# Kernel optimization log

Measured on AMD Instinct MI355X. Metric: run time of the kernel, lower is better.

The kernel has to match this reference:

```python
import jax, jax.numpy as jnp
import numpy as np

SOFTMAX_TEMP = 0.01  # config['networks']['matcher_block']['softmax_temp']
B, WINDOW, C, N, WIDTH = 2, 2, 64, 400, 256


def setup_inputs() -> dict:
    key = jax.random.key(0)
    k1, k2, k3 = jax.random.split(key, 3)
    BW = B * WINDOW
    keypoint_scores = jax.random.uniform(k1, (BW, 1, N), dtype=jnp.float32)
    keypoint_desc = jax.random.normal(k2, (BW, C, N), dtype=jnp.float32)
    desc_dense = jax.random.normal(k3, (BW, C, WIDTH, WIDTH), dtype=jnp.float32)
    # pairing indices exactly as built in SoftmaxRefMatcher.__init__
    tgt_ids, src_ids = [], []
    for b in range(B):
        for w in range(WINDOW - 1):
            for t in range(w + 1, WINDOW):
                src_ids.append(w + b * WINDOW)
                tgt_ids.append(t + b * WINDOW)
    return {
        "keypoint_scores": keypoint_scores,
        "keypoint_desc": keypoint_desc,
        "desc_dense": desc_dense,
        "tgt_ids": jnp.array(tgt_ids, dtype=jnp.int32),
        "src_ids": jnp.array(src_ids, dtype=jnp.int32),
    }


def _l2_normalize(x):
    # F.normalize(x, dim=1), eps=1e-12
    return x / jnp.maximum(jnp.linalg.norm(x, axis=1, keepdims=True), 1e-12)


def reference(keypoint_scores, keypoint_desc, desc_dense, tgt_ids, src_ids):
    BW, Cdim, H, W = desc_dense.shape
    HW = H * W
    # src_coords_dense: meshgrid('ij') -> coords[k] = (u=k%W, v=k//W)
    hw = jnp.arange(HW)
    coords = jnp.stack([(hw % W).astype(jnp.float32),
                        (hw // W).astype(jnp.float32)], axis=1)  # [HW, 2]

    src_desc = _l2_normalize(desc_dense.reshape(BW, Cdim, HW))[src_ids]  # [P, C, HW]
    tgt_desc = _l2_normalize(keypoint_desc)[tgt_ids]                     # [P, C, N]

    match_vals = jnp.einsum('pcn,pcm->pnm', tgt_desc, src_desc)          # [P, N, HW]
    soft_match = jax.nn.softmax(match_vals / SOFTMAX_TEMP, axis=2)
    pseudo_coords = jnp.einsum('pnm,mk->pnk', soft_match, coords)        # [P, N, 2]

    tgt_scores = keypoint_scores[tgt_ids]
    return pseudo_coords, tgt_scores, tgt_ids, src_ids
```

## Files before the change

### kernel.cpp

```cpp
#include <hip/hip_runtime.h>
#include <math.h>

#define NPAIR  2
#define KDIM   64
#define NKP    400
#define NTILE  28
#define HWPIX  65536
#define MREF   70.0f
#define LOG2E  1.44269504f

#define BFRAG_DW (NPAIR*NTILE*2*2*256)

using frag_ab = __attribute__((ext_vector_type(8))) short;
using f32x4   = __attribute__((ext_vector_type(4))) float;

__device__ __forceinline__ unsigned short f2bf(float f){
    unsigned u = __builtin_bit_cast(unsigned, f);
    u += 0x7fffu + ((u >> 16) & 1u);
    return (unsigned short)(u >> 16);
}
__device__ __forceinline__ float bf2f(unsigned short h){
    unsigned u = ((unsigned)h) << 16;
    return __builtin_bit_cast(float, u);
}

__global__ __launch_bounds__(256) void prep_kernel(
    const float* __restrict__ ksc, const float* __restrict__ kd,
    const int* __restrict__ tgt_ids, const int* __restrict__ src_ids,
    unsigned* __restrict__ wsu, float* __restrict__ out)
{
    __shared__ float xs[KDIM][33];
    __shared__ float inv_s[32];
    int d = blockIdx.x, p = blockIdx.y, t = threadIdx.x;
    int tgt = tgt_ids[p];
    int nl = t & 31, c0 = t >> 5;
    #pragma unroll
    for (int cc = 0; cc < 8; ++cc){
        int c = cc*8 + c0;
        int n = d*32 + nl;
        xs[c][nl] = (n < NKP) ? kd[(tgt*KDIM + c)*NKP + n] : 0.f;
    }
    __syncthreads();
    if (t < 32){
        float s = 0.f;
        #pragma unroll
        for (int c = 0; c < KDIM; ++c){ float v = xs[c][t]; s = fmaf(v, v, s); }
        inv_s[t] = 1.f / fmaxf(sqrtf(s), 1e-12f);
    }
    __syncthreads();
    {
        int l = t & 63, rk = t >> 6;
        int rt = rk >> 1, ks = rk & 1;
        int cl = l & 15, g = l >> 4;
        int nloc = rt*16 + cl;
        float inv = inv_s[nloc];
        int k0 = ks*32 + g*8;
        unsigned hu[4], lu[4];
        #pragma unroll
        for (int j2 = 0; j2 < 4; ++j2){
            float xa = xs[k0 + 2*j2    ][nloc] * inv;
            float xb = xs[k0 + 2*j2 + 1][nloc] * inv;
            unsigned short ha = f2bf(xa), hb = f2bf(xb);
            unsigned short la = f2bf(xa - bf2f(ha)), lb = f2bf(xb - bf2f(hb));
            hu[j2] = (unsigned)ha | ((unsigned)hb << 16);
            lu[j2] = (unsigned)la | ((unsigned)lb << 16);
        }
        int nt = d*2 + rt;
        unsigned base = (unsigned)(((p*NTILE + nt)*2 + ks)*2)*256 + l*4;
        *(uint4*)&wsu[base]       = make_uint4(hu[0], hu[1], hu[2], hu[3]);
        *(uint4*)&wsu[base + 256] = make_uint4(lu[0], lu[1], lu[2], lu[3]);
    }
    if (t < 32){
        int n = d*32 + t;
        if (n < NKP) out[NPAIR*NKP*2 + p*NKP + n] = ksc[tgt*NKP + n];
    }
    if (d == 0 && t == 0){
        out[NPAIR*NKP*3 + p]         = (float)tgt;
        out[NPAIR*NKP*3 + NPAIR + p] = (float)src_ids[p];
    }
}

__global__ __launch_bounds__(256, 4) void match_kernel(
    const float* __restrict__ dd, const int* __restrict__ src_ids,
    const unsigned* __restrict__ wsu, float* __restrict__ part)
{
    __shared__ unsigned lds[8192];
    __shared__ float ssp[256];
    __shared__ float invn_s[128];
    int mb = blockIdx.x, p = blockIdx.y, t = threadIdx.x;
    int w = t >> 6, l = t & 63;
    int g = l >> 4;

    const unsigned* wB = wsu + (unsigned)p*28672 + (unsigned)l*4;
    uint4 Bb0[4], Bb1[4];
    #pragma unroll
    for (int k = 0; k < 4; ++k) Bb0[k] = *(const uint4*)(wB + k*256);
    #pragma unroll
    for (int k = 0; k < 4; ++k) Bb1[k] = *(const uint4*)(wB + 1024 + k*256);

    const float* plane = dd + (size_t)src_ids[p]*KDIM*HWPIX + mb*128;

    {
        int m = t & 127, kh = t >> 7;
        unsigned sw = (unsigned)(m & 7);
        float ssum = 0.f;
        const float* cp = plane + m + (size_t)kh*32*HWPIX;
        #pragma unroll
        for (int s2l = 0; s2l < 4; ++s2l){
            float v[8];
            #pragma unroll
            for (int j = 0; j < 8; ++j) v[j] = cp[(size_t)(s2l*8 + j)*HWPIX];
            unsigned hq[4], lq[4];
            #pragma unroll
            for (int q = 0; q < 4; ++q){
                float a = v[2*q], b = v[2*q+1];
                ssum = fmaf(a, a, ssum);
                ssum = fmaf(b, b, ssum);
                unsigned ta = (__builtin_bit_cast(unsigned, a) + 0x8000u) & 0xFFFF0000u;
                unsigned tb = (__builtin_bit_cast(unsigned, b) + 0x8000u) & 0xFFFF0000u;
                float la = a - __builtin_bit_cast(float, ta);
                float lb = b - __builtin_bit_cast(float, tb);
                hq[q] = __builtin_amdgcn_perm(tb, ta, 0x07060302u);
                lq[q] = __builtin_amdgcn_perm(__builtin_bit_cast(unsigned, lb),
                                              __builtin_bit_cast(unsigned, la), 0x07060302u);
            }
            unsigned slot = ((unsigned)(kh*4 + s2l)) ^ sw;
            unsigned dwb = (unsigned)m*32 + slot*4;
            *(uint4*)&lds[dwb]        = make_uint4(hq[0], hq[1], hq[2], hq[3]);
            *(uint4*)&lds[4096 + dwb] = make_uint4(lq[0], lq[1], lq[2], lq[3]);
        }
        ssp[t] = ssum;
    }
    __syncthreads();
    if (t < 128)
        invn_s[t] = (100.f * LOG2E) / fmaxf(sqrtf(ssp[t] + ssp[t + 128]), 1e-12f);
    __syncthreads();

    int mloc0 = w*32;
    uint4 Ac[2][4];
    #pragma unroll
    for (int mt = 0; mt < 2; ++mt){
        unsigned m = (unsigned)(mloc0 + mt*16 + (l & 15));
        unsigned sw = m & 7;
        #pragma unroll
        for (int k = 0; k < 4; ++k){
            unsigned slot = (((unsigned)(k >> 1))*4 + (unsigned)g) ^ sw;
            Ac[mt][k] = *(const uint4*)&lds[(unsigned)(k & 1)*4096 + m*32 + slot*4];
        }
    }
    __syncthreads();

    const float mref2 = MREF * LOG2E;
    float invm8[2][4], ub_[2];
    #pragma unroll
    for (int mt = 0; mt < 2; ++mt){
        ub_[mt] = (float)(mloc0 + mt*16 + g*4);
        #pragma unroll
        for (int r = 0; r < 4; ++r)
            invm8[mt][r] = invn_s[mloc0 + mt*16 + g*4 + r];
    }

    f32x4 acc0[2], acc1[2];
    float* wp = (float*)lds;

    auto zacc = [&](f32x4* a){
        a[0] = (f32x4){0.f,0.f,0.f,0.f};
        a[1] = (f32x4){0.f,0.f,0.f,0.f};
    };
    auto unit = [&](const uint4* Bq, f32x4* a2){
        #pragma unroll
        for (int ks = 0; ks < 2; ++ks){
            frag_ab bH  = __builtin_bit_cast(frag_ab, Bq[ks*2]);
            frag_ab bL  = __builtin_bit_cast(frag_ab, Bq[ks*2 + 1]);
            frag_ab a0H = __builtin_bit_cast(frag_ab, Ac[0][ks*2]);
            frag_ab a0L = __builtin_bit_cast(frag_ab, Ac[0][ks*2 + 1]);
            frag_ab a1H = __builtin_bit_cast(frag_ab, Ac[1][ks*2]);
            frag_ab a1L = __builtin_bit_cast(frag_ab, Ac[1][ks*2 + 1]);
            a2[0] = __builtin_amdgcn_mfma_f32_16x16x32_bf16(a0H, bH, a2[0], 0, 0, 0);
            a2[1] = __builtin_amdgcn_mfma_f32_16x16x32_bf16(a1H, bH, a2[1], 0, 0, 0);
            a2[0] = __builtin_amdgcn_mfma_f32_16x16x32_bf16(a0H, bL, a2[0], 0, 0, 0);
            a2[1] = __builtin_amdgcn_mfma_f32_16x16x32_bf16(a1H, bL, a2[1], 0, 0, 0);
            a2[0] = __builtin_amdgcn_mfma_f32_16x16x32_bf16(a0L, bH, a2[0], 0, 0, 0);
            a2[1] = __builtin_amdgcn_mfma_f32_16x16x32_bf16(a1L, bH, a2[1], 0, 0, 0);
        }
    };
    auto loadB = [&](int nt, uint4* B){
        const unsigned* q = wB + (unsigned)nt*1024;
        #pragma unroll
        for (int k = 0; k < 4; ++k) B[k] = *(const uint4*)(q + k*256);
    };
    auto epi = [&](const f32x4* a2, int nt){
        float Ssum = 0.f, Usum = 0.f;
        #pragma unroll
        for (int mt = 0; mt < 2; ++mt){
            float e0 = __builtin_amdgcn_exp2f(fmaf(a2[mt][0], invm8[mt][0], -mref2));
            float e1 = __builtin_amdgcn_exp2f(fmaf(a2[mt][1], invm8[mt][1], -mref2));
            float e2 = __builtin_amdgcn_exp2f(fmaf(a2[mt][2], invm8[mt][2], -mref2));
            float e3 = __builtin_amdgcn_exp2f(fmaf(a2[mt][3], invm8[mt][3], -mref2));
            float Sm = (e0 + e1) + (e2 + e3);
            float Um = fmaf(e2, 2.f, e1);
            Um = fmaf(e3, 3.f, Um);
            Um = fmaf(ub_[mt], Sm, Um);
            Ssum += Sm; Usum += Um;
        }
        Ssum += __shfl_xor(Ssum, 16); Usum += __shfl_xor(Usum, 16);
        Ssum += __shfl_xor(Ssum, 32); Usum += __shfl_xor(Usum, 32);
        if (l < 16)
            *(float2*)&wp[((unsigned)(w*NTILE + nt)*16 + (unsigned)l)*2] =
                make_float2(Ssum, Usum);
    };

    zacc(acc0); unit(Bb0, acc0);
    #pragma unroll 1
    for (int j = 0; j < 13; ++j){
        loadB(2*j + 2, Bb0);
        zacc(acc1); unit(Bb1, acc1);
        epi(acc0, 2*j);
        loadB(2*j + 3, Bb1);
        zacc(acc0); unit(Bb0, acc0);
        epi(acc1, 2*j + 1);
    }
    zacc(acc1); unit(Bb1, acc1);
    epi(acc0, 26);
    epi(acc1, 27);

    __syncthreads();
    for (int idx = t; idx < NTILE*16; idx += 256){
        int nt = idx >> 4, cl = idx & 15;
        float S = 0.f, U = 0.f;
        #pragma unroll
        for (int ww = 0; ww < 4; ++ww){
            float2 q = *(const float2*)&wp[((unsigned)(ww*NTILE + nt)*16 + (unsigned)cl)*2];
            S += q.x; U += q.y;
        }
        *(float2*)&part[(((size_t)p*NTILE + nt)*512 + mb)*32 + cl*2] =
            make_float2(S, U);
    }
}

__global__ __launch_bounds__(256) void merge_kernel(
    const float* __restrict__ part, float* __restrict__ out)
{
    __shared__ float red[3][4][16];
    int nt = blockIdx.x, p = blockIdx.y, t = threadIdx.x;
    int j = t & 15, mb0 = t >> 4;
    const float* base = part + ((size_t)(p*NTILE + nt)*512)*32;
    float S = 0.f, U = 0.f, V = 0.f;
    #pragma unroll 4
    for (int k = 0; k < 32; ++k){
        int mbk = mb0 + k*16;
        float2 q = *(const float2*)&base[(mbk*16 + j)*2];
        S += q.x;
        U += q.y + (float)((mbk & 1)*128)*q.x;
        V = fmaf((float)(mbk >> 1), q.x, V);
    }
    S += __shfl_xor(S, 16); U += __shfl_xor(U, 16); V += __shfl_xor(V, 16);
    S += __shfl_xor(S, 32); U += __shfl_xor(U, 32); V += __shfl_xor(V, 32);
    int w = t >> 6, l = t & 63;
    if (l < 16){ red[0][w][j] = S; red[1][w][j] = U; red[2][w][j] = V; }
    __syncthreads();
    if (t < 16){
        float Sf = red[0][0][t] + red[0][1][t] + red[0][2][t] + red[0][3][t];
        float Uf = red[1][0][t] + red[1][1][t] + red[1][2][t] + red[1][3][t];
        float Vf = red[2][0][t] + red[2][1][t] + red[2][2][t] + red[2][3][t];
        int n = nt*16 + t;
        out[(p*NKP + n)*2 + 0] = Uf / Sf;
        out[(p*NKP + n)*2 + 1] = Vf / Sf;
    }
}

extern "C" void kernel_launch(void* const* d_in, const int* in_sizes, int n_in,
                              void* d_out, int out_size, void* d_ws, size_t ws_size,
                              hipStream_t stream)
{
    const float* ksc     = (const float*)d_in[0];
    const float* kd      = (const float*)d_in[1];
    const float* dd      = (const float*)d_in[2];
    const int*   tgt_ids = (const int*)d_in[3];
    const int*   src_ids = (const int*)d_in[4];
    float* out = (float*)d_out;
    unsigned* wsu = (unsigned*)d_ws;
    float* part = (float*)d_ws + BFRAG_DW;

    prep_kernel <<<dim3(14, NPAIR),  256, 0, stream>>>(ksc, kd, tgt_ids, src_ids, wsu, out);
    match_kernel<<<dim3(512, NPAIR), 256, 0, stream>>>(dd, src_ids, wsu, part);
    merge_kernel<<<dim3(25, NPAIR),  256, 0, stream>>>(part, out);
}
```

Baseline: 127.0 us.

## Double pixels per match block so each B fragment load feeds four M tiles

Each match block now covers 256 pixels (one full image row) instead of 128. Each wave holds four 16-row A tiles instead of two, so every B fragment loaded from the workspace is reused across twice as many MFMAs. The number of blocks and partial sums halves, and the merge kernel is simplified to match the new row-per-block indexing. In exchange, register pressure rises (launch bounds drop to 2 blocks per SIMD), occupancy falls, and the grid shrinks to 512 blocks total, which may reduce latency hiding on the HBM-bound load phase.

```diff
diff --git a/kernel.cpp b/kernel.cpp
--- a/kernel.cpp
+++ b/kernel.cpp
@@ -8,6 +8,7 @@
 #define HWPIX  65536
 #define MREF   70.0f
 #define LOG2E  1.44269504f
+#define MBLK   256
 
 #define BFRAG_DW (NPAIR*NTILE*2*2*256)
 
@@ -80,13 +81,13 @@
     }
 }
 
-__global__ __launch_bounds__(256, 4) void match_kernel(
+__global__ __launch_bounds__(256, 2) void match_kernel(
     const float* __restrict__ dd, const int* __restrict__ src_ids,
     const unsigned* __restrict__ wsu, float* __restrict__ part)
 {
     __shared__ unsigned lds[8192];
     __shared__ float ssp[256];
-    __shared__ float invn_s[128];
+    __shared__ float invn_s[256];
     int mb = blockIdx.x, p = blockIdx.y, t = threadIdx.x;
     int w = t >> 6, l = t & 63;
     int g = l >> 4;
@@ -98,13 +99,15 @@
     #pragma unroll
     for (int k = 0; k < 4; ++k) Bb1[k] = *(const uint4*)(wB + 1024 + k*256);
 
-    const float* plane = dd + (size_t)src_ids[p]*KDIM*HWPIX + mb*128;
-
-    {
-        int m = t & 127, kh = t >> 7;
+    const float* plane = dd + (size_t)src_ids[p]*KDIM*HWPIX + (size_t)mb*256;
+
+    uint4 Ac[4][4];
+    int m = t & 127, kh = t >> 7;
+    #pragma unroll
+    for (int chunk = 0; chunk < 2; ++chunk){
         unsigned sw = (unsigned)(m & 7);
         float ssum = 0.f;
-        const float* cp = plane + m + (size_t)kh*32*HWPIX;
+        const float* cp = plane + chunk*128 + m + (size_t)kh*32*HWPIX;
         #pragma unroll
         for (int s2l = 0; s2l < 4; ++s2l){
             float v[8];
@@ -130,58 +133,64 @@
             *(uint4*)&lds[4096 + dwb] = make_uint4(lq[0], lq[1], lq[2], lq[3]);
         }
         ssp[t] = ssum;
-    }
-    __syncthreads();
-    if (t < 128)
-        invn_s[t] = (100.f * LOG2E) / fmaxf(sqrtf(ssp[t] + ssp[t + 128]), 1e-12f);
-    __syncthreads();
-
-    int mloc0 = w*32;
-    uint4 Ac[2][4];
-    #pragma unroll
-    for (int mt = 0; mt < 2; ++mt){
-        unsigned m = (unsigned)(mloc0 + mt*16 + (l & 15));
-        unsigned sw = m & 7;
-        #pragma unroll
-        for (int k = 0; k < 4; ++k){
-            unsigned slot = (((unsigned)(k >> 1))*4 + (unsigned)g) ^ sw;
-            Ac[mt][k] = *(const uint4*)&lds[(unsigned)(k & 1)*4096 + m*32 + slot*4];
-        }
-    }
-    __syncthreads();
+        __syncthreads();
+        if (t < 128)
+            invn_s[chunk*128 + t] =
+                (100.f * LOG2E) / fmaxf(sqrtf(ssp[t] + ssp[t + 128]), 1e-12f);
+        if ((w >> 1) == chunk){
+            int lw = (w & 1)*64;
+            #pragma unroll
+            for (int mt = 0; mt < 4; ++mt){
+                unsigned mm = (unsigned)(lw + mt*16 + (l & 15));
+                unsigned sw2 = mm & 7;
+                #pragma unroll
+                for (int k = 0; k < 4; ++k){
+                    unsigned slot = (((unsigned)(k >> 1))*4 + (unsigned)g) ^ sw2;
+                    Ac[mt][k] = *(const uint4*)&lds[(unsigned)(k & 1)*4096 + mm*32 + slot*4];
+                }
+            }
+        }
+        __syncthreads();
+    }
 
     const float mref2 = MREF * LOG2E;
-    float invm8[2][4], ub_[2];
-    #pragma unroll
-    for (int mt = 0; mt < 2; ++mt){
+    float invm8[4][4], ub_[4];
+    int mloc0 = w*64;
+    #pragma unroll
+    for (int mt = 0; mt < 4; ++mt){
         ub_[mt] = (float)(mloc0 + mt*16 + g*4);
         #pragma unroll
         for (int r = 0; r < 4; ++r)
             invm8[mt][r] = invn_s[mloc0 + mt*16 + g*4 + r];
     }
 
-    f32x4 acc0[2], acc1[2];
+    f32x4 acc0[4], acc1[4];
     float* wp = (float*)lds;
 
     auto zacc = [&](f32x4* a){
-        a[0] = (f32x4){0.f,0.f,0.f,0.f};
-        a[1] = (f32x4){0.f,0.f,0.f,0.f};
-    };
-    auto unit = [&](const uint4* Bq, f32x4* a2){
+        #pragma unroll
+        for (int mt = 0; mt < 4; ++mt) a[mt] = (f32x4){0.f,0.f,0.f,0.f};
+    };
+    auto unit = [&](const uint4* Bq, f32x4* a4){
         #pragma unroll
         for (int ks = 0; ks < 2; ++ks){
-            frag_ab bH  = __builtin_bit_cast(frag_ab, Bq[ks*2]);
-            frag_ab bL  = __builtin_bit_cast(frag_ab, Bq[ks*2 + 1]);
-            frag_ab a0H = __builtin_bit_cast(frag_ab, Ac[0][ks*2]);
-            frag_ab a0L = __builtin_bit_cast(frag_ab, Ac[0][ks*2 + 1]);
-            frag_ab a1H = __builtin_bit_cast(frag_ab, Ac[1][ks*2]);
-            frag_ab a1L = __builtin_bit_cast(frag_ab, Ac[1][ks*2 + 1]);
-            a2[0] = __builtin_amdgcn_mfma_f32_16x16x32_bf16(a0H, bH, a2[0], 0, 0, 0);
-            a2[1] = __builtin_amdgcn_mfma_f32_16x16x32_bf16(a1H, bH, a2[1], 0, 0, 0);
-            a2[0] = __builtin_amdgcn_mfma_f32_16x16x32_bf16(a0H, bL, a2[0], 0, 0, 0);
-            a2[1] = __builtin_amdgcn_mfma_f32_16x16x32_bf16(a1H, bL, a2[1], 0, 0, 0);
-            a2[0] = __builtin_amdgcn_mfma_f32_16x16x32_bf16(a0L, bH, a2[0], 0, 0, 0);
-            a2[1] = __builtin_amdgcn_mfma_f32_16x16x32_bf16(a1L, bH, a2[1], 0, 0, 0);
+            frag_ab bH = __builtin_bit_cast(frag_ab, Bq[ks*2]);
+            frag_ab bL = __builtin_bit_cast(frag_ab, Bq[ks*2 + 1]);
+            #pragma unroll
+            for (int mt = 0; mt < 4; ++mt){
+                frag_ab aH = __builtin_bit_cast(frag_ab, Ac[mt][ks*2]);
+                a4[mt] = __builtin_amdgcn_mfma_f32_16x16x32_bf16(aH, bH, a4[mt], 0, 0, 0);
+            }
+            #pragma unroll
+            for (int mt = 0; mt < 4; ++mt){
+                frag_ab aH = __builtin_bit_cast(frag_ab, Ac[mt][ks*2]);
+                a4[mt] = __builtin_amdgcn_mfma_f32_16x16x32_bf16(aH, bL, a4[mt], 0, 0, 0);
+            }
+            #pragma unroll
+            for (int mt = 0; mt < 4; ++mt){
+                frag_ab aL = __builtin_bit_cast(frag_ab, Ac[mt][ks*2 + 1]);
+                a4[mt] = __builtin_amdgcn_mfma_f32_16x16x32_bf16(aL, bH, a4[mt], 0, 0, 0);
+            }
         }
     };
     auto loadB = [&](int nt, uint4* B){
@@ -189,14 +198,14 @@
         #pragma unroll
         for (int k = 0; k < 4; ++k) B[k] = *(const uint4*)(q + k*256);
     };
-    auto epi = [&](const f32x4* a2, int nt){
+    auto epi = [&](const f32x4* a4, int nt){
         float Ssum = 0.f, Usum = 0.f;
         #pragma unroll
-        for (int mt = 0; mt < 2; ++mt){
-            float e0 = __builtin_amdgcn_exp2f(fmaf(a2[mt][0], invm8[mt][0], -mref2));
-            float e1 = __builtin_amdgcn_exp2f(fmaf(a2[mt][1], invm8[mt][1], -mref2));
-            float e2 = __builtin_amdgcn_exp2f(fmaf(a2[mt][2], invm8[mt][2], -mref2));
-            float e3 = __builtin_amdgcn_exp2f(fmaf(a2[mt][3], invm8[mt][3], -mref2));
+        for (int mt = 0; mt < 4; ++mt){
+            float e0 = __builtin_amdgcn_exp2f(fmaf(a4[mt][0], invm8[mt][0], -mref2));
+            float e1 = __builtin_amdgcn_exp2f(fmaf(a4[mt][1], invm8[mt][1], -mref2));
+            float e2 = __builtin_amdgcn_exp2f(fmaf(a4[mt][2], invm8[mt][2], -mref2));
+            float e3 = __builtin_amdgcn_exp2f(fmaf(a4[mt][3], invm8[mt][3], -mref2));
             float Sm = (e0 + e1) + (e2 + e3);
             float Um = fmaf(e2, 2.f, e1);
             Um = fmaf(e3, 3.f, Um);
@@ -212,13 +221,13 @@
 
     zacc(acc0); unit(Bb0, acc0);
     #pragma unroll 1
-    for (int j = 0; j < 13; ++j){
-        loadB(2*j + 2, Bb0);
+    for (int jj = 0; jj < 13; ++jj){
+        loadB(2*jj + 2, Bb0);
         zacc(acc1); unit(Bb1, acc1);
-        epi(acc0, 2*j);
-        loadB(2*j + 3, Bb1);
+        epi(acc0, 2*jj);
+        loadB(2*jj + 3, Bb1);
         zacc(acc0); unit(Bb0, acc0);
-        epi(acc1, 2*j + 1);
+        epi(acc1, 2*jj + 1);
     }
     zacc(acc1); unit(Bb1, acc1);
     epi(acc0, 26);
@@ -233,7 +242,7 @@
             float2 q = *(const float2*)&wp[((unsigned)(ww*NTILE + nt)*16 + (unsigned)cl)*2];
             S += q.x; U += q.y;
         }
-        *(float2*)&part[(((size_t)p*NTILE + nt)*512 + mb)*32 + cl*2] =
+        *(float2*)&part[(((size_t)p*NTILE + nt)*MBLK + mb)*32 + cl*2] =
             make_float2(S, U);
     }
 }
@@ -244,15 +253,15 @@
     __shared__ float red[3][4][16];
     int nt = blockIdx.x, p = blockIdx.y, t = threadIdx.x;
     int j = t & 15, mb0 = t >> 4;
-    const float* base = part + ((size_t)(p*NTILE + nt)*512)*32;
+    const float* base = part + (size_t)(p*NTILE + nt)*MBLK*32;
     float S = 0.f, U = 0.f, V = 0.f;
     #pragma unroll 4
-    for (int k = 0; k < 32; ++k){
+    for (int k = 0; k < 16; ++k){
         int mbk = mb0 + k*16;
         float2 q = *(const float2*)&base[(mbk*16 + j)*2];
         S += q.x;
-        U += q.y + (float)((mbk & 1)*128)*q.x;
-        V = fmaf((float)(mbk >> 1), q.x, V);
+        U += q.y;
+        V = fmaf((float)mbk, q.x, V);
     }
     S += __shfl_xor(S, 16); U += __shfl_xor(U, 16); V += __shfl_xor(V, 16);
     S += __shfl_xor(S, 32); U += __shfl_xor(U, 32); V += __shfl_xor(V, 32);
@@ -282,7 +291,7 @@
     unsigned* wsu = (unsigned*)d_ws;
     float* part = (float*)d_ws + BFRAG_DW;
 
-    prep_kernel <<<dim3(14, NPAIR),  256, 0, stream>>>(ksc, kd, tgt_ids, src_ids, wsu, out);
-    match_kernel<<<dim3(512, NPAIR), 256, 0, stream>>>(dd, src_ids, wsu, part);
-    merge_kernel<<<dim3(25, NPAIR),  256, 0, stream>>>(part, out);
-}
+    prep_kernel <<<dim3(14, NPAIR),   256, 0, stream>>>(ksc, kd, tgt_ids, src_ids, wsu, out);
+    match_kernel<<<dim3(MBLK, NPAIR), 256, 0, stream>>>(dd, src_ids, wsu, part);
+    merge_kernel<<<dim3(25, NPAIR),   256, 0, stream>>>(part, out);
+}
```

Result: no change. 126.0 us (-0.8%).
